# Performance work log

Hardware: AMD Instinct MI355X
Metric: run time of the kernel (lower is better)

## Reference

```python
import jax, jax.numpy as jnp
import numpy as np
from math import sqrt

D_MODEL = 1024
N_HEADS = 16
FF_MULT = 4
MAX_DIST = 512
LN_EPS = 1e-5


def layer_norm(x, g, b):
    mu = jnp.mean(x, axis=-1, keepdims=True)
    var = jnp.var(x, axis=-1, keepdims=True)
    return (x - mu) * jax.lax.rsqrt(var + LN_EPS) * g + b


def setup_inputs() -> dict:
    key = jax.random.key(0)
    ks = jax.random.split(key, 10)
    D, H, F = D_MODEL, N_HEADS, D_MODEL * FF_MULT
    s = 0.02
    return {
        "x": jax.random.normal(ks[0], (2, 2048, D), dtype=jnp.float32),
        "w_qkv": jax.random.normal(ks[1], (D, 3 * D), dtype=jnp.float32) * s,
        "b_qkv": jnp.zeros((3 * D,), jnp.float32),
        "w_out": jax.random.normal(ks[2], (D, D), dtype=jnp.float32) * s,
        "b_out": jnp.zeros((D,), jnp.float32),
        "rel_bias": jax.random.normal(ks[3], (2 * MAX_DIST + 1, H), dtype=jnp.float32) * s,
        "g1": jnp.ones((D,), jnp.float32),
        "beta1": jnp.zeros((D,), jnp.float32),
        "w1": jax.random.normal(ks[4], (D, F), dtype=jnp.float32) * s,
        "b1": jnp.zeros((F,), jnp.float32),
        "w2": jax.random.normal(ks[5], (F, D), dtype=jnp.float32) * s,
        "b2": jnp.zeros((D,), jnp.float32),
        "g2": jnp.ones((D,), jnp.float32),
        "beta2": jnp.zeros((D,), jnp.float32),
    }


def reference(x, w_qkv, b_qkv, w_out, b_out, rel_bias, g1, beta1, w1, b1, w2, b2, g2, beta2):
    B, T, D = x.shape
    H = N_HEADS
    hd = D // H
    qkv = x @ w_qkv + b_qkv                      # [B,T,3D]
    q, k, v = jnp.split(qkv, 3, axis=-1)
    # [B,H,T,hd]
    q = q.reshape(B, T, H, hd).transpose(0, 2, 1, 3)
    k = k.reshape(B, T, H, hd).transpose(0, 2, 1, 3)
    v = v.reshape(B, T, H, hd).transpose(0, 2, 1, 3)
    scores = jnp.einsum("bhqd,bhkd->bhqk", q, k) / sqrt(hd)
    # relative position bias: gather from table [2*max_dist+1, H]
    rel = jnp.clip(jnp.arange(T)[None, :] - jnp.arange(T)[:, None], -MAX_DIST, MAX_DIST) + MAX_DIST
    bias = rel_bias[rel].transpose(2, 0, 1)       # [H,T,T]
    attn = jax.nn.softmax(scores + bias[None], axis=-1)
    out = jnp.einsum("bhqk,bhkd->bhqd", attn, v).transpose(0, 2, 1, 3).reshape(B, T, D)
    out = out @ w_out + b_out                     # dropout inactive (eval)
    x2 = layer_norm(x + out, g1, beta1)
    ff = jax.nn.gelu(x2 @ w1 + b1, approximate=False) @ w2 + b2
    x3 = layer_norm(x2 + ff, g2, beta2)
    return (x3, attn)
```

## Files before the change

### kernel.cpp

```cpp
#include <hip/hip_runtime.h>
#include <hip/hip_bf16.h>
#include <cstdint>
#include <cstddef>

#define DEVFN static __device__ __forceinline__

typedef __attribute__((ext_vector_type(8))) short bf16x8;
typedef __attribute__((ext_vector_type(4))) float f32x4;

#define WAITVM(N) asm volatile("s_waitcnt vmcnt(" #N ")" ::: "memory")
#define WAITLGKM() asm volatile("s_waitcnt lgkmcnt(0)" ::: "memory")
#define BAR() __builtin_amdgcn_s_barrier()

DEVFN float exp2f_fast(float x) { return __builtin_amdgcn_exp2f(x); }

DEVFN ushort f2bf(float f) {
  uint32_t u = __float_as_uint(f);
  return (ushort)((u + 0x7fffu + ((u >> 16) & 1u)) >> 16);
}

DEVFN void gl_lds16(const void* g, void* l) {
  __builtin_amdgcn_global_load_lds(
      (const __attribute__((address_space(1))) void*)g,
      (__attribute__((address_space(3))) void*)l, 16, 0, 0);
}

DEVFN float wred_sum(float v) {
#pragma unroll
  for (int o = 32; o; o >>= 1) v += __shfl_xor(v, o);
  return v;
}


__global__ __launch_bounds__(256) void pack_bf16(const float* __restrict__ in,
                                                 ushort* __restrict__ out) {
  size_t i = ((size_t)blockIdx.x * 256 + threadIdx.x) * 4;
  float4 v = *(const float4*)&in[i];
  ushort4 u = make_ushort4(f2bf(v.x), f2bf(v.y), f2bf(v.z), f2bf(v.w));
  *(ushort4*)&out[i] = u;
}

__global__ __launch_bounds__(256) void wtrans(const float* __restrict__ in,
                                              ushort* __restrict__ out,
                                              int K, int N) {
  __shared__ float tile[32][33];
  int n0 = blockIdx.x * 32, k0 = blockIdx.y * 32;
  int tid = threadIdx.x;
#pragma unroll
  for (int i = 0; i < 4; ++i) {
    int idx = tid + i * 256;
    int r = idx >> 5, c = idx & 31;
    tile[r][c] = in[(size_t)(k0 + r) * N + n0 + c];
  }
  __syncthreads();
#pragma unroll
  for (int i = 0; i < 4; ++i) {
    int idx = tid + i * 256;
    int r = idx >> 5, c = idx & 31;
    out[(size_t)(n0 + r) * K + k0 + c] = f2bf(tile[c][r]);
  }
}

__global__ __launch_bounds__(256) void pack_vT(const ushort* __restrict__ qkv,
                                               ushort* __restrict__ vT) {
  __shared__ ushort tile[64][72];
  int bh = blockIdx.y, b = bh >> 4, h = bh & 15;
  int t0 = blockIdx.x * 64;
  int tid = threadIdx.x;
#pragma unroll
  for (int i = 0; i < 16; ++i) {
    int idx = tid + i * 256;
    int r = idx >> 6, c = idx & 63;
    tile[r][c] = qkv[(size_t)(b * 2048 + t0 + r) * 3072 + 2048 + h * 64 + c];
  }
  __syncthreads();
#pragma unroll
  for (int i = 0; i < 16; ++i) {
    int idx = tid + i * 256;
    int d = idx >> 6, t = idx & 63;
    vT[((size_t)bh * 64 + d) * 2048 + t0 + t] = tile[t][d];
  }
}


template <bool GELU, bool STF32, bool STBF16>
__global__ __launch_bounds__(256)
void gemm128(const ushort* __restrict__ A, int lda,
             const ushort* __restrict__ BT, int ldb,
             const float* __restrict__ bias,
             float* __restrict__ Cf, ushort* __restrict__ Cb, int ldc, int K) {
  __shared__ ushort lsa[128 * 64];
  __shared__ ushort lsb[128 * 64];
  const int tid = threadIdx.x;
  const int lane = tid & 63;
  const int wv = tid >> 6;
  const int wr = (wv >> 1) * 64, wc = (wv & 1) * 64;
  const ushort* Ab = A + (size_t)blockIdx.y * 128 * lda;
  const ushort* Bb = BT + (size_t)blockIdx.x * 128 * ldb;
  f32x4 acc[4][4] = {};
  int rowS[4], slotS[4];
#pragma unroll
  for (int i = 0; i < 4; ++i) {
    int idx = tid + i * 256;
    rowS[i] = idx >> 3;
    slotS[i] = (idx & 7) ^ (rowS[i] & 7);
  }
  for (int kt = 0; kt < K; kt += 64) {
    __syncthreads();
#pragma unroll
    for (int i = 0; i < 4; ++i) {
      gl_lds16(Ab + (size_t)rowS[i] * lda + kt + slotS[i] * 8, &lsa[(tid + i * 256) * 8]);
      gl_lds16(Bb + (size_t)rowS[i] * ldb + kt + slotS[i] * 8, &lsb[(tid + i * 256) * 8]);
    }
    asm volatile("s_waitcnt vmcnt(0)" ::: "memory");
    __syncthreads();
#pragma unroll
    for (int kk = 0; kk < 2; ++kk) {
      bf16x8 af[4], bfr[4];
      const int g = kk * 4 + (lane >> 4);
#pragma unroll
      for (int m = 0; m < 4; ++m) {
        int r = wr + m * 16 + (lane & 15);
        af[m] = *(const bf16x8*)&lsa[r * 64 + ((g ^ (r & 7)) * 8)];
      }
#pragma unroll
      for (int n = 0; n < 4; ++n) {
        int r = wc + n * 16 + (lane & 15);
        bfr[n] = *(const bf16x8*)&lsb[r * 64 + ((g ^ (r & 7)) * 8)];
      }
#pragma unroll
      for (int m = 0; m < 4; ++m)
#pragma unroll
        for (int n = 0; n < 4; ++n)
          acc[m][n] = __builtin_amdgcn_mfma_f32_16x16x32_bf16(af[m], bfr[n], acc[m][n], 0, 0, 0);
    }
  }
  const int rb = blockIdx.y * 128 + wr + ((lane >> 4) << 2);
  const int cb = blockIdx.x * 128 + wc + (lane & 15);
#pragma unroll
  for (int m = 0; m < 4; ++m)
#pragma unroll
    for (int n = 0; n < 4; ++n) {
      int col = cb + n * 16;
      float bv = bias[col];
#pragma unroll
      for (int i = 0; i < 4; ++i) {
        int row = rb + m * 16 + i;
        float v = acc[m][n][i] + bv;
        if (GELU) v = 0.5f * v * (1.0f + erff(v * 0.70710678f));
        if (STF32) Cf[(size_t)row * ldc + col] = v;
        if (STBF16) Cb[(size_t)row * ldc + col] = f2bf(v);
      }
    }
}


__global__ __launch_bounds__(256, 2)
void attn_fused(const ushort* __restrict__ qkv, const ushort* __restrict__ vT,
                const float* __restrict__ rel_bias,
                float* __restrict__ attn, ushort* __restrict__ ctx) {
  __shared__ ushort lsq[128 * 64];
  __shared__ ushort lsk[2][64 * 64];
  __shared__ ushort lsv[2][64 * 64];
  __shared__ ushort lsp[128 * 64];
  __shared__ float extb[1034];
  const int tid = threadIdx.x;
  const int lane = tid & 63;
  const int wv = tid >> 6;
  const int hi = lane >> 4;
  const int lo = lane & 15;
  const int bh = blockIdx.y, b = bh >> 4, h = bh & 15;
  const int q0 = blockIdx.x * 128;
  const ushort* qp = qkv + (size_t)b * 2048 * 3072 + h * 64;
  const ushort* kp = qp + 1024;
  const ushort* vp = vT + (size_t)bh * 64 * 2048;
  float* attnb = attn + (size_t)bh * 2048 * 2048;
  const float C_SC = 0.18033688011f;

  for (int i = tid; i < 1034; i += 256) {
    int j = i - 3;
    j = j < 0 ? 0 : (j > 1024 ? 1024 : j);
    extb[i] = rel_bias[j * 16 + h] * 1.44269504f;
  }

#pragma unroll
  for (int i = 0; i < 4; ++i) {
    int idx = tid + i * 256;
    int row = idx >> 3;
    int slot = (idx & 7) ^ (row & 7);
    gl_lds16(qp + (size_t)(q0 + row) * 3072 + slot * 8, &lsq[idx * 8]);
  }
  WAITVM(0);
  WAITLGKM();
  BAR();

  bf16x8 qf[2][2];
#pragma unroll
  for (int mq = 0; mq < 2; ++mq)
#pragma unroll
    for (int kk = 0; kk < 2; ++kk) {
      int r = wv * 32 + mq * 16 + lo;
      int g = kk * 4 + hi;
      qf[mq][kk] = *(const bf16x8*)&lsq[r * 64 + ((g ^ (r & 7)) * 8)];
    }

  const int r0 = tid >> 3;
  const int sl0 = (tid & 7) ^ (r0 & 7);
  const int r1 = (tid + 256) >> 3;
  const int sl1 = ((tid + 256) & 7) ^ (r1 & 7);

  auto stageK = [&](int t, int buf) {
    gl_lds16(kp + (size_t)(t * 64 + r0) * 3072 + sl0 * 8, &lsk[buf][tid * 8]);
    gl_lds16(kp + (size_t)(t * 64 + r1) * 3072 + sl1 * 8, &lsk[buf][(tid + 256) * 8]);
  };
  auto stageV = [&](int t, int buf) {
    gl_lds16(vp + (size_t)r0 * 2048 + t * 64 + sl0 * 8, &lsv[buf][tid * 8]);
    gl_lds16(vp + (size_t)r1 * 2048 + t * 64 + sl1 * 8, &lsv[buf][(tid + 256) * 8]);
  };

  auto mfmaS = [&](int buf, f32x4 sacc[4][2]) {
    __builtin_amdgcn_s_setprio(1);
#pragma unroll
    for (int kk = 0; kk < 2; ++kk) {
      const int g = kk * 4 + hi;
      bf16x8 ak[4];
#pragma unroll
      for (int mk = 0; mk < 4; ++mk) {
        int r = mk * 16 + lo;
        ak[mk] = *(const bf16x8*)&lsk[buf][r * 64 + ((g ^ (r & 7)) * 8)];
      }
#pragma unroll
      for (int mk = 0; mk < 4; ++mk)
#pragma unroll
        for (int mq = 0; mq < 2; ++mq)
          sacc[mk][mq] =
              __builtin_amdgcn_mfma_f32_16x16x32_bf16(ak[mk], qf[mq][kk], sacc[mk][mq], 0, 0, 0);
    }
    __builtin_amdgcn_s_setprio(0);
  };

  float l_part[2] = {0.0f, 0.0f};
  stageK(0, 0);
  for (int t = 0; t < 32; ++t) {
    if (t < 31) {
      stageK(t + 1, (t + 1) & 1);
      WAITVM(2);
    } else {
      WAITVM(0);
    }
    BAR();
    f32x4 sacc[4][2] = {};
    mfmaS(t & 1, sacc);
    const bool farR = (t * 64) >= q0 + 640;
    const bool farL = (t * 64 + 63) <= q0 - 512;
    if (farR || farL) {
      const float bc = farR ? extb[3 + 1024] : extb[3];
#pragma unroll
      for (int mq = 0; mq < 2; ++mq) {
        float s = 0.0f;
#pragma unroll
        for (int mk = 0; mk < 4; ++mk)
#pragma unroll
          for (int i = 0; i < 4; ++i)
            s += exp2f_fast(fmaf(sacc[mk][mq][i], C_SC, bc));
        l_part[mq] += s;
      }
    } else {
      const int kbase = t * 64 + hi * 4;
      const int qr = q0 + wv * 32 + lo;
#pragma unroll
      for (int mq = 0; mq < 2; ++mq) {
        float s = 0.0f;
#pragma unroll
        for (int mk = 0; mk < 4; ++mk) {
          int k0 = (kbase + mk * 16) - (qr + mq * 16) + 515;
          k0 = k0 < 0 ? 0 : (k0 > 1030 ? 1030 : k0);
#pragma unroll
          for (int i = 0; i < 4; ++i)
            s += exp2f_fast(fmaf(sacc[mk][mq][i], C_SC, extb[k0 + i]));
        }
        l_part[mq] += s;
      }
    }
    BAR();
  }

  float inv_l[2];
#pragma unroll
  for (int mq = 0; mq < 2; ++mq) {
    float l = l_part[mq];
    l += __shfl_xor(l, 16);
    l += __shfl_xor(l, 32);
    inv_l[mq] = 1.0f / l;
  }

  f32x4 acc_o[2][4] = {};
  stageK(0, 0);
  stageV(0, 0);
  for (int t = 0; t < 32; ++t) {
    if (t < 31) {
      stageK(t + 1, (t + 1) & 1);
      stageV(t + 1, (t + 1) & 1);
    }
    if (t == 0) { WAITVM(4); }
    else if (t < 31) { WAITVM(12); }
    else { WAITVM(8); }
    BAR();
    f32x4 sacc[4][2] = {};
    mfmaS(t & 1, sacc);
    const bool farT = ((t * 64) >= q0 + 640) || ((t * 64 + 63) <= q0 - 512);
    const float bcf = ((t * 64) >= q0 + 640) ? extb[3 + 1024] : extb[3];
#pragma unroll
    for (int mq = 0; mq < 2; ++mq) {
      const int row = wv * 32 + mq * 16 + lo;
      const float il = inv_l[mq];
#pragma unroll
      for (int mk = 0; mk < 4; ++mk) {
        const int c0 = mk * 16 + hi * 4;
        float p4[4];
        if (farT) {
#pragma unroll
          for (int i = 0; i < 4; ++i)
            p4[i] = exp2f_fast(fmaf(sacc[mk][mq][i], C_SC, bcf)) * il;
        } else {
          int k0 = (t * 64 + c0) - (q0 + row) + 515;
          k0 = k0 < 0 ? 0 : (k0 > 1030 ? 1030 : k0);
#pragma unroll
          for (int i = 0; i < 4; ++i)
            p4[i] = exp2f_fast(fmaf(sacc[mk][mq][i], C_SC, extb[k0 + i])) * il;
        }
        ushort4 u = make_ushort4(f2bf(p4[0]), f2bf(p4[1]), f2bf(p4[2]), f2bf(p4[3]));
        *(ushort4*)&lsp[row * 64 + (((c0 >> 3) ^ (row & 7)) << 3) + (c0 & 7)] = u;
        *(float4*)&attnb[(size_t)(q0 + row) * 2048 + t * 64 + c0] =
            make_float4(p4[0], p4[1], p4[2], p4[3]);
      }
    }
    WAITLGKM();
    BAR();
    __builtin_amdgcn_s_setprio(1);
#pragma unroll
    for (int kk = 0; kk < 2; ++kk) {
      const int g = kk * 4 + hi;
      bf16x8 ap[2], bv2[4];
#pragma unroll
      for (int m = 0; m < 2; ++m) {
        int r = wv * 32 + m * 16 + lo;
        ap[m] = *(const bf16x8*)&lsp[r * 64 + ((g ^ (r & 7)) * 8)];
      }
#pragma unroll
      for (int n = 0; n < 4; ++n) {
        int r = n * 16 + lo;
        bv2[n] = *(const bf16x8*)&lsv[t & 1][r * 64 + ((g ^ (r & 7)) * 8)];
      }
#pragma unroll
      for (int m = 0; m < 2; ++m)
#pragma unroll
        for (int n = 0; n < 4; ++n)
          acc_o[m][n] = __builtin_amdgcn_mfma_f32_16x16x32_bf16(ap[m], bv2[n], acc_o[m][n], 0, 0, 0);
    }
    __builtin_amdgcn_s_setprio(0);
  }

#pragma unroll
  for (int m = 0; m < 2; ++m)
#pragma unroll
    for (int n = 0; n < 4; ++n) {
      int col = h * 64 + n * 16 + lo;
#pragma unroll
      for (int i = 0; i < 4; ++i) {
        int row = q0 + wv * 32 + m * 16 + (hi << 2) + i;
        ctx[(size_t)(b * 2048 + row) * 1024 + col] = f2bf(acc_o[m][n][i]);
      }
    }
}


__global__ __launch_bounds__(256)
void add_ln(const float* __restrict__ a, const float* __restrict__ r,
            const float* __restrict__ g, const float* __restrict__ be,
            float* __restrict__ outf, ushort* __restrict__ outb) {
  const int tid = threadIdx.x;
  const size_t base = (size_t)blockIdx.x * 1024 + tid * 4;
  float4 va = *(const float4*)&a[base];
  float4 vr = *(const float4*)&r[base];
  float x0 = va.x + vr.x, x1 = va.y + vr.y, x2 = va.z + vr.z, x3 = va.w + vr.w;
  float s = x0 + x1 + x2 + x3;
  float s2 = x0 * x0 + x1 * x1 + x2 * x2 + x3 * x3;
  s = wred_sum(s);
  s2 = wred_sum(s2);
  __shared__ float rs[4], rq[4];
  if ((tid & 63) == 0) { rs[tid >> 6] = s; rq[tid >> 6] = s2; }
  __syncthreads();
  s = rs[0] + rs[1] + rs[2] + rs[3];
  s2 = rq[0] + rq[1] + rq[2] + rq[3];
  const float mean = s * (1.0f / 1024.0f);
  const float var = s2 * (1.0f / 1024.0f) - mean * mean;
  const float sc = rsqrtf(var + 1e-5f);
  float4 vg = *(const float4*)&g[tid * 4];
  float4 vb = *(const float4*)&be[tid * 4];
  float y0 = (x0 - mean) * sc * vg.x + vb.x;
  float y1 = (x1 - mean) * sc * vg.y + vb.y;
  float y2 = (x2 - mean) * sc * vg.z + vb.z;
  float y3 = (x3 - mean) * sc * vg.w + vb.w;
  *(float4*)&outf[base] = make_float4(y0, y1, y2, y3);
  if (outb) {
    ushort4 u = make_ushort4(f2bf(y0), f2bf(y1), f2bf(y2), f2bf(y3));
    *(ushort4*)&outb[base] = u;
  }
}


extern "C" void kernel_launch(void* const* d_in, const int* in_sizes, int n_in,
                              void* d_out, int out_size, void* d_ws, size_t ws_size,
                              hipStream_t stream) {
  const float* x     = (const float*)d_in[0];
  const float* w_qkv = (const float*)d_in[1];
  const float* b_qkv = (const float*)d_in[2];
  const float* w_out = (const float*)d_in[3];
  const float* b_out = (const float*)d_in[4];
  const float* relb  = (const float*)d_in[5];
  const float* g1    = (const float*)d_in[6];
  const float* be1   = (const float*)d_in[7];
  const float* w1    = (const float*)d_in[8];
  const float* b1    = (const float*)d_in[9];
  const float* w2    = (const float*)d_in[10];
  const float* b2    = (const float*)d_in[11];
  const float* g2    = (const float*)d_in[12];
  const float* be2   = (const float*)d_in[13];

  float* x3o  = (float*)d_out;
  float* attn = x3o + (size_t)4194304;

  char* w = (char*)d_ws;
  size_t off = 0;
  auto alloc = [&](size_t bytes) {
    void* p = w + off;
    off += (bytes + 255) & ~(size_t)255;
    return p;
  };
  ushort* x_bf   = (ushort*)alloc(4096ull * 1024 * 2);
  ushort* wqkvT  = (ushort*)alloc(3072ull * 1024 * 2);
  ushort* woutT  = (ushort*)alloc(1024ull * 1024 * 2);
  ushort* w1T    = (ushort*)alloc(4096ull * 1024 * 2);
  ushort* w2T    = (ushort*)alloc(1024ull * 4096 * 2);
  ushort* qkv_bf = (ushort*)alloc(4096ull * 3072 * 2);
  ushort* vT     = (ushort*)alloc(32ull * 64 * 2048 * 2);
  ushort* ctx_bf = (ushort*)alloc(4096ull * 1024 * 2);
  float*  projf  = (float*)alloc(4096ull * 1024 * 4);
  float*  x2f    = (float*)alloc(4096ull * 1024 * 4);
  ushort* x2bf   = (ushort*)alloc(4096ull * 1024 * 2);
  ushort* ff1_bf = (ushort*)alloc(4096ull * 4096 * 2);
  float*  ff2f   = projf;

  pack_bf16<<<4096, 256, 0, stream>>>(x, x_bf);
  wtrans<<<dim3(96, 32), 256, 0, stream>>>(w_qkv, wqkvT, 1024, 3072);
  wtrans<<<dim3(32, 32), 256, 0, stream>>>(w_out, woutT, 1024, 1024);
  wtrans<<<dim3(128, 32), 256, 0, stream>>>(w1, w1T, 1024, 4096);
  wtrans<<<dim3(32, 128), 256, 0, stream>>>(w2, w2T, 4096, 1024);

  gemm128<false, false, true><<<dim3(24, 32), 256, 0, stream>>>(
      x_bf, 1024, wqkvT, 1024, b_qkv, nullptr, qkv_bf, 3072, 1024);
  pack_vT<<<dim3(32, 32), 256, 0, stream>>>(qkv_bf, vT);
  attn_fused<<<dim3(16, 32), 256, 0, stream>>>(qkv_bf, vT, relb, attn, ctx_bf);

  gemm128<false, true, false><<<dim3(8, 32), 256, 0, stream>>>(
      ctx_bf, 1024, woutT, 1024, b_out, projf, nullptr, 1024, 1024);
  add_ln<<<4096, 256, 0, stream>>>(x, projf, g1, be1, x2f, x2bf);
  gemm128<true, false, true><<<dim3(32, 32), 256, 0, stream>>>(
      x2bf, 1024, w1T, 1024, b1, nullptr, ff1_bf, 4096, 1024);
  gemm128<false, true, false><<<dim3(8, 32), 256, 0, stream>>>(
      ff1_bf, 4096, w2T, 4096, b2, ff2f, nullptr, 1024, 4096);
  add_ln<<<4096, 256, 0, stream>>>(x2f, ff2f, g2, be2, x3o, nullptr);
}
```

Measured before the change: 502.4 us.

## Split fused attention into denominator pass and PV pass kernels

Splits the two-pass fused attention kernel into a separate kernel that computes the softmax denominators (writing inverse row sums to a workspace buffer) and a second kernel that recomputes the scores, writes probabilities and does PV. The Q staging buffer is aliased onto existing LDS (K buffers in the first kernel, P buffer in the second), and launch bounds are raised to 4 and 3 blocks per CU. The aim is more occupancy and less LDS per block, at the cost of an extra launch, an extra Q load and a small global round trip for the inverse sums.

```diff
diff --git a/kernel.cpp b/kernel.cpp
--- a/kernel.cpp
+++ b/kernel.cpp
@@ -155,11 +155,136 @@
 }
 
 
-__global__ __launch_bounds__(256, 2)
-void attn_fused(const ushort* __restrict__ qkv, const ushort* __restrict__ vT,
-                const float* __restrict__ rel_bias,
-                float* __restrict__ attn, ushort* __restrict__ ctx) {
-  __shared__ ushort lsq[128 * 64];
+__global__ __launch_bounds__(256, 4)
+void attn_den(const ushort* __restrict__ qkv, const float* __restrict__ rel_bias,
+              float* __restrict__ invl) {
+  __shared__ ushort lsk[2][64 * 64];
+  __shared__ float extb[1034];
+  const int tid = threadIdx.x;
+  const int lane = tid & 63;
+  const int wv = tid >> 6;
+  const int hi = lane >> 4;
+  const int lo = lane & 15;
+  const int bh = blockIdx.y, b = bh >> 4, h = bh & 15;
+  const int q0 = blockIdx.x * 128;
+  const ushort* qp = qkv + (size_t)b * 2048 * 3072 + h * 64;
+  const ushort* kp = qp + 1024;
+  const float C_SC = 0.18033688011f;
+  ushort* lsq = (ushort*)lsk;
+
+  for (int i = tid; i < 1034; i += 256) {
+    int j = i - 3;
+    j = j < 0 ? 0 : (j > 1024 ? 1024 : j);
+    extb[i] = rel_bias[j * 16 + h] * 1.44269504f;
+  }
+#pragma unroll
+  for (int i = 0; i < 4; ++i) {
+    int idx = tid + i * 256;
+    int row = idx >> 3;
+    int slot = (idx & 7) ^ (row & 7);
+    gl_lds16(qp + (size_t)(q0 + row) * 3072 + slot * 8, &lsq[idx * 8]);
+  }
+  WAITVM(0);
+  WAITLGKM();
+  BAR();
+  bf16x8 qf[2][2];
+#pragma unroll
+  for (int mq = 0; mq < 2; ++mq)
+#pragma unroll
+    for (int kk = 0; kk < 2; ++kk) {
+      int r = wv * 32 + mq * 16 + lo;
+      int g = kk * 4 + hi;
+      qf[mq][kk] = *(const bf16x8*)&lsq[r * 64 + ((g ^ (r & 7)) * 8)];
+    }
+  WAITLGKM();
+  BAR();
+
+  const int r0 = tid >> 3;
+  const int sl0 = (tid & 7) ^ (r0 & 7);
+  const int r1 = (tid + 256) >> 3;
+  const int sl1 = ((tid + 256) & 7) ^ (r1 & 7);
+  auto stageK = [&](int t, int buf) {
+    gl_lds16(kp + (size_t)(t * 64 + r0) * 3072 + sl0 * 8, &lsk[buf][tid * 8]);
+    gl_lds16(kp + (size_t)(t * 64 + r1) * 3072 + sl1 * 8, &lsk[buf][(tid + 256) * 8]);
+  };
+
+  float l_part[2] = {0.0f, 0.0f};
+  stageK(0, 0);
+  for (int t = 0; t < 32; ++t) {
+    if (t < 31) {
+      stageK(t + 1, (t + 1) & 1);
+      WAITVM(2);
+    } else {
+      WAITVM(0);
+    }
+    BAR();
+    f32x4 sacc[4][2] = {};
+    __builtin_amdgcn_s_setprio(1);
+#pragma unroll
+    for (int kk = 0; kk < 2; ++kk) {
+      const int g = kk * 4 + hi;
+      bf16x8 ak[4];
+#pragma unroll
+      for (int mk = 0; mk < 4; ++mk) {
+        int r = mk * 16 + lo;
+        ak[mk] = *(const bf16x8*)&lsk[t & 1][r * 64 + ((g ^ (r & 7)) * 8)];
+      }
+#pragma unroll
+      for (int mk = 0; mk < 4; ++mk)
+#pragma unroll
+        for (int mq = 0; mq < 2; ++mq)
+          sacc[mk][mq] =
+              __builtin_amdgcn_mfma_f32_16x16x32_bf16(ak[mk], qf[mq][kk], sacc[mk][mq], 0, 0, 0);
+    }
+    __builtin_amdgcn_s_setprio(0);
+    const bool farR = (t * 64) >= q0 + 640;
+    const bool farL = (t * 64 + 63) <= q0 - 512;
+    if (farR || farL) {
+      const float bc = farR ? extb[3 + 1024] : extb[3];
+#pragma unroll
+      for (int mq = 0; mq < 2; ++mq) {
+        float s = 0.0f;
+#pragma unroll
+        for (int mk = 0; mk < 4; ++mk)
+#pragma unroll
+          for (int i = 0; i < 4; ++i)
+            s += exp2f_fast(fmaf(sacc[mk][mq][i], C_SC, bc));
+        l_part[mq] += s;
+      }
+    } else {
+      const int kbase = t * 64 + hi * 4;
+      const int qr = q0 + wv * 32 + lo;
+#pragma unroll
+      for (int mq = 0; mq < 2; ++mq) {
+        float s = 0.0f;
+#pragma unroll
+        for (int mk = 0; mk < 4; ++mk) {
+          int k0 = (kbase + mk * 16) - (qr + mq * 16) + 515;
+          k0 = k0 < 0 ? 0 : (k0 > 1030 ? 1030 : k0);
+#pragma unroll
+          for (int i = 0; i < 4; ++i)
+            s += exp2f_fast(fmaf(sacc[mk][mq][i], C_SC, extb[k0 + i]));
+        }
+        l_part[mq] += s;
+      }
+    }
+    BAR();
+  }
+
+#pragma unroll
+  for (int mq = 0; mq < 2; ++mq) {
+    float l = l_part[mq];
+    l += __shfl_xor(l, 16);
+    l += __shfl_xor(l, 32);
+    if (hi == 0)
+      invl[(size_t)bh * 2048 + q0 + wv * 32 + mq * 16 + lo] = 1.0f / l;
+  }
+}
+
+__global__ __launch_bounds__(256, 3)
+void attn_pv2(const ushort* __restrict__ qkv, const ushort* __restrict__ vT,
+              const float* __restrict__ rel_bias, const float* __restrict__ invl,
+              float* __restrict__ attn, ushort* __restrict__ ctx) {
   __shared__ ushort lsk[2][64 * 64];
   __shared__ ushort lsv[2][64 * 64];
   __shared__ ushort lsp[128 * 64];
@@ -182,18 +307,16 @@
     j = j < 0 ? 0 : (j > 1024 ? 1024 : j);
     extb[i] = rel_bias[j * 16 + h] * 1.44269504f;
   }
-
 #pragma unroll
   for (int i = 0; i < 4; ++i) {
     int idx = tid + i * 256;
     int row = idx >> 3;
     int slot = (idx & 7) ^ (row & 7);
-    gl_lds16(qp + (size_t)(q0 + row) * 3072 + slot * 8, &lsq[idx * 8]);
+    gl_lds16(qp + (size_t)(q0 + row) * 3072 + slot * 8, &lsp[idx * 8]);
   }
   WAITVM(0);
   WAITLGKM();
   BAR();
-
   bf16x8 qf[2][2];
 #pragma unroll
   for (int mq = 0; mq < 2; ++mq)
@@ -201,14 +324,20 @@
     for (int kk = 0; kk < 2; ++kk) {
       int r = wv * 32 + mq * 16 + lo;
       int g = kk * 4 + hi;
-      qf[mq][kk] = *(const bf16x8*)&lsq[r * 64 + ((g ^ (r & 7)) * 8)];
-    }
+      qf[mq][kk] = *(const bf16x8*)&lsp[r * 64 + ((g ^ (r & 7)) * 8)];
+    }
+  WAITLGKM();
+  BAR();
+
+  float il[2];
+#pragma unroll
+  for (int mq = 0; mq < 2; ++mq)
+    il[mq] = invl[(size_t)bh * 2048 + q0 + wv * 32 + mq * 16 + lo];
 
   const int r0 = tid >> 3;
   const int sl0 = (tid & 7) ^ (r0 & 7);
   const int r1 = (tid + 256) >> 3;
   const int sl1 = ((tid + 256) & 7) ^ (r1 & 7);
-
   auto stageK = [&](int t, int buf) {
     gl_lds16(kp + (size_t)(t * 64 + r0) * 3072 + sl0 * 8, &lsk[buf][tid * 8]);
     gl_lds16(kp + (size_t)(t * 64 + r1) * 3072 + sl1 * 8, &lsk[buf][(tid + 256) * 8]);
@@ -218,82 +347,6 @@
     gl_lds16(vp + (size_t)r1 * 2048 + t * 64 + sl1 * 8, &lsv[buf][(tid + 256) * 8]);
   };
 
-  auto mfmaS = [&](int buf, f32x4 sacc[4][2]) {
-    __builtin_amdgcn_s_setprio(1);
-#pragma unroll
-    for (int kk = 0; kk < 2; ++kk) {
-      const int g = kk * 4 + hi;
-      bf16x8 ak[4];
-#pragma unroll
-      for (int mk = 0; mk < 4; ++mk) {
-        int r = mk * 16 + lo;
-        ak[mk] = *(const bf16x8*)&lsk[buf][r * 64 + ((g ^ (r & 7)) * 8)];
-      }
-#pragma unroll
-      for (int mk = 0; mk < 4; ++mk)
-#pragma unroll
-        for (int mq = 0; mq < 2; ++mq)
-          sacc[mk][mq] =
-              __builtin_amdgcn_mfma_f32_16x16x32_bf16(ak[mk], qf[mq][kk], sacc[mk][mq], 0, 0, 0);
-    }
-    __builtin_amdgcn_s_setprio(0);
-  };
-
-  float l_part[2] = {0.0f, 0.0f};
-  stageK(0, 0);
-  for (int t = 0; t < 32; ++t) {
-    if (t < 31) {
-      stageK(t + 1, (t + 1) & 1);
-      WAITVM(2);
-    } else {
-      WAITVM(0);
-    }
-    BAR();
-    f32x4 sacc[4][2] = {};
-    mfmaS(t & 1, sacc);
-    const bool farR = (t * 64) >= q0 + 640;
-    const bool farL = (t * 64 + 63) <= q0 - 512;
-    if (farR || farL) {
-      const float bc = farR ? extb[3 + 1024] : extb[3];
-#pragma unroll
-      for (int mq = 0; mq < 2; ++mq) {
-        float s = 0.0f;
-#pragma unroll
-        for (int mk = 0; mk < 4; ++mk)
-#pragma unroll
-          for (int i = 0; i < 4; ++i)
-            s += exp2f_fast(fmaf(sacc[mk][mq][i], C_SC, bc));
-        l_part[mq] += s;
-      }
-    } else {
-      const int kbase = t * 64 + hi * 4;
-      const int qr = q0 + wv * 32 + lo;
-#pragma unroll
-      for (int mq = 0; mq < 2; ++mq) {
-        float s = 0.0f;
-#pragma unroll
-        for (int mk = 0; mk < 4; ++mk) {
-          int k0 = (kbase + mk * 16) - (qr + mq * 16) + 515;
-          k0 = k0 < 0 ? 0 : (k0 > 1030 ? 1030 : k0);
-#pragma unroll
-          for (int i = 0; i < 4; ++i)
-            s += exp2f_fast(fmaf(sacc[mk][mq][i], C_SC, extb[k0 + i]));
-        }
-        l_part[mq] += s;
-      }
-    }
-    BAR();
-  }
-
-  float inv_l[2];
-#pragma unroll
-  for (int mq = 0; mq < 2; ++mq) {
-    float l = l_part[mq];
-    l += __shfl_xor(l, 16);
-    l += __shfl_xor(l, 32);
-    inv_l[mq] = 1.0f / l;
-  }
-
   f32x4 acc_o[2][4] = {};
   stageK(0, 0);
   stageV(0, 0);
@@ -307,13 +360,31 @@
     else { WAITVM(8); }
     BAR();
     f32x4 sacc[4][2] = {};
-    mfmaS(t & 1, sacc);
-    const bool farT = ((t * 64) >= q0 + 640) || ((t * 64 + 63) <= q0 - 512);
-    const float bcf = ((t * 64) >= q0 + 640) ? extb[3 + 1024] : extb[3];
+    __builtin_amdgcn_s_setprio(1);
+#pragma unroll
+    for (int kk = 0; kk < 2; ++kk) {
+      const int g = kk * 4 + hi;
+      bf16x8 ak[4];
+#pragma unroll
+      for (int mk = 0; mk < 4; ++mk) {
+        int r = mk * 16 + lo;
+        ak[mk] = *(const bf16x8*)&lsk[t & 1][r * 64 + ((g ^ (r & 7)) * 8)];
+      }
+#pragma unroll
+      for (int mk = 0; mk < 4; ++mk)
+#pragma unroll
+        for (int mq = 0; mq < 2; ++mq)
+          sacc[mk][mq] =
+              __builtin_amdgcn_mfma_f32_16x16x32_bf16(ak[mk], qf[mq][kk], sacc[mk][mq], 0, 0, 0);
+    }
+    __builtin_amdgcn_s_setprio(0);
+    const bool farR = (t * 64) >= q0 + 640;
+    const bool farT = farR || ((t * 64 + 63) <= q0 - 512);
+    const float bcf = farR ? extb[3 + 1024] : extb[3];
 #pragma unroll
     for (int mq = 0; mq < 2; ++mq) {
       const int row = wv * 32 + mq * 16 + lo;
-      const float il = inv_l[mq];
+      const float l = il[mq];
 #pragma unroll
       for (int mk = 0; mk < 4; ++mk) {
         const int c0 = mk * 16 + hi * 4;
@@ -321,13 +392,13 @@
         if (farT) {
 #pragma unroll
           for (int i = 0; i < 4; ++i)
-            p4[i] = exp2f_fast(fmaf(sacc[mk][mq][i], C_SC, bcf)) * il;
+            p4[i] = exp2f_fast(fmaf(sacc[mk][mq][i], C_SC, bcf)) * l;
         } else {
           int k0 = (t * 64 + c0) - (q0 + row) + 515;
           k0 = k0 < 0 ? 0 : (k0 > 1030 ? 1030 : k0);
 #pragma unroll
           for (int i = 0; i < 4; ++i)
-            p4[i] = exp2f_fast(fmaf(sacc[mk][mq][i], C_SC, extb[k0 + i])) * il;
+            p4[i] = exp2f_fast(fmaf(sacc[mk][mq][i], C_SC, extb[k0 + i])) * l;
         }
         ushort4 u = make_ushort4(f2bf(p4[0]), f2bf(p4[1]), f2bf(p4[2]), f2bf(p4[3]));
         *(ushort4*)&lsp[row * 64 + (((c0 >> 3) ^ (row & 7)) << 3) + (c0 & 7)] = u;
@@ -446,6 +517,7 @@
   ushort* qkv_bf = (ushort*)alloc(4096ull * 3072 * 2);
   ushort* vT     = (ushort*)alloc(32ull * 64 * 2048 * 2);
   ushort* ctx_bf = (ushort*)alloc(4096ull * 1024 * 2);
+  float*  invl   = (float*)alloc(32ull * 2048 * 4);
   float*  projf  = (float*)alloc(4096ull * 1024 * 4);
   float*  x2f    = (float*)alloc(4096ull * 1024 * 4);
   ushort* x2bf   = (ushort*)alloc(4096ull * 1024 * 2);
@@ -460,8 +532,9 @@
 
   gemm128<false, false, true><<<dim3(24, 32), 256, 0, stream>>>(
       x_bf, 1024, wqkvT, 1024, b_qkv, nullptr, qkv_bf, 3072, 1024);
+  attn_den<<<dim3(16, 32), 256, 0, stream>>>(qkv_bf, relb, invl);
   pack_vT<<<dim3(32, 32), 256, 0, stream>>>(qkv_bf, vT);
-  attn_fused<<<dim3(16, 32), 256, 0, stream>>>(qkv_bf, vT, relb, attn, ctx_bf);
+  attn_pv2<<<dim3(16, 32), 256, 0, stream>>>(qkv_bf, vT, relb, invl, attn, ctx_bf);
 
   gemm128<false, true, false><<<dim3(8, 32), 256, 0, stream>>>(
       ctx_bf, 1024, woutT, 1024, b_out, projf, nullptr, 1024, 1024);
```

New measurement: 511.1 us. About the same (+1.7%).
